# Optimization experiments

Hardware: AMD Instinct MI355X
Metric: run time of the kernel (lower is better)

The kernel has to match this reference:

```python
import jax, jax.numpy as jnp
import numpy as np

B, T, C = 2, 2048, 1024
H = 16
D = C // H  # head_dim = 64


def setup_inputs() -> dict:
    key = jax.random.key(0)
    k1, k2, k3 = jax.random.split(key, 3)
    x = jax.random.normal(k1, (B, T, C), dtype=jnp.float32)
    # torch Linear(C, 3C, bias=False): y = x @ W.T; store transposed weight [C, 3C]
    w_qkv = jax.random.normal(k2, (C, 3 * C), dtype=jnp.float32) * (1.0 / np.sqrt(C))
    w_out = jax.random.normal(k3, (C, C), dtype=jnp.float32) * (1.0 / np.sqrt(C))
    return {"x": x, "w_qkv": w_qkv, "w_out": w_out}


def reference(x, w_qkv, w_out):
    b, t, c = x.shape
    qkv = jnp.einsum('btc,cd->btd', x, w_qkv)          # [B,T,3C]
    q, k, v = jnp.split(qkv, 3, axis=-1)
    # [B,T,C] -> [B,H,T,D]
    def heads(u):
        return u.reshape(b, t, H, D).transpose(0, 2, 1, 3)
    q, k, v = heads(q), heads(k), heads(v)
    scale = 1.0 / np.sqrt(D)
    attn = jnp.einsum('bhqd,bhkd->bhqk', q, k) * scale  # [B,H,T,T]
    causal = jnp.tril(jnp.ones((t, t), dtype=bool))
    attn = jnp.where(causal, attn, -jnp.inf)
    attn = jax.nn.softmax(attn, axis=-1)                # dropout p=0.0 -> identity
    out = jnp.einsum('bhqk,bhkd->bhqd', attn, v)        # [B,H,T,D]
    out = out.transpose(0, 2, 1, 3).reshape(b, t, c)
    return jnp.einsum('btc,co->bto', out, w_out)
```

## Files before the change

kernel.cpp:

```cpp
#include <hip/hip_runtime.h>
#include <hip/hip_bf16.h>
#include <stdint.h>


#define Bv 2
#define Tv 2048
#define Cv 1024
#define Hv 16
#define Dv 64
#define Mv 4096

typedef __attribute__((ext_vector_type(8))) __bf16 bf16x8;
typedef __attribute__((ext_vector_type(4))) __bf16 bf16x4;
typedef __attribute__((ext_vector_type(4))) float f32x4;
typedef __attribute__((ext_vector_type(4))) unsigned short ushort4v;

__device__ __forceinline__ unsigned short f2bs(float f) {
  union { __bf16 h; unsigned short s; } u;
  u.h = (__bf16)f;
  return u.s;
}

__device__ __forceinline__ void gload16(const void* g, void* l) {
  __builtin_amdgcn_global_load_lds(
      (__attribute__((address_space(1))) void*)(uintptr_t)g,
      (__attribute__((address_space(3))) void*)(unsigned int)(uintptr_t)l,
      16, 0, 0);
}

__device__ __forceinline__ bf16x8 ldfrag(const unsigned short* p) {
  return *reinterpret_cast<const bf16x8*>(p);
}
__device__ __forceinline__ bf16x8 ldfragb(const __bf16* p) {
  return *reinterpret_cast<const bf16x8*>(p);
}

__global__ void __launch_bounds__(256) cast_bf16(const float* __restrict__ in,
                                                 unsigned short* __restrict__ out) {
  int i = (blockIdx.x * 256 + threadIdx.x) * 8;
  float4 a = *reinterpret_cast<const float4*>(in + i);
  float4 b = *reinterpret_cast<const float4*>(in + i + 4);
  ushort4v o0, o1;
  o0.x = f2bs(a.x); o0.y = f2bs(a.y); o0.z = f2bs(a.z); o0.w = f2bs(a.w);
  o1.x = f2bs(b.x); o1.y = f2bs(b.y); o1.z = f2bs(b.z); o1.w = f2bs(b.w);
  *reinterpret_cast<ushort4v*>(out + i) = o0;
  *reinterpret_cast<ushort4v*>(out + i + 4) = o1;
}

__global__ void __launch_bounds__(256) transcast(const float* __restrict__ in,
                                                 unsigned short* __restrict__ out,
                                                 int R, int Cc) {
  __shared__ float tile[32][33];
  int c0 = blockIdx.x * 32;
  int r0 = blockIdx.y * 32;
  int tc = threadIdx.x & 31, tr = threadIdx.x >> 5;
#pragma unroll
  for (int i = 0; i < 4; i++)
    tile[tr + i * 8][tc] = in[(size_t)(r0 + tr + i * 8) * Cc + c0 + tc];
  __syncthreads();
#pragma unroll
  for (int i = 0; i < 4; i++)
    out[(size_t)(c0 + tr + i * 8) * R + r0 + tc] = f2bs(tile[tc][tr + i * 8]);
}

template <int EPI>
__global__ void __launch_bounds__(256) gemm128(
    const unsigned short* __restrict__ A, const unsigned short* __restrict__ Bt,
    float* __restrict__ outF, unsigned short* __restrict__ qo,
    unsigned short* __restrict__ ko, unsigned short* __restrict__ vTo, int N) {
  __shared__ unsigned short la[3][4][128][8];
  __shared__ unsigned short lb[3][4][128][8];
  const int K = 1024;
  const int NT = K / 32;
  int mb = blockIdx.y * 128, nb = blockIdx.x * 128;
  int tid = threadIdx.x;
  int l = tid & 63, w = tid >> 6;
  int wr = w >> 1, wc = w & 1;
  int lr = l & 15, lg = l >> 4;
  f32x4 acc[4][4] = {};
  int c0 = tid >> 7, r0 = tid & 127;

  auto STAGE = [&](int t, int buf) {
    int kb = t * 32;
    gload16(A + (size_t)(mb + r0) * K + kb + c0 * 8, &la[buf][c0][r0][0]);
    gload16(A + (size_t)(mb + r0) * K + kb + (c0 + 2) * 8, &la[buf][c0 + 2][r0][0]);
    gload16(Bt + (size_t)(nb + r0) * K + kb + c0 * 8, &lb[buf][c0][r0][0]);
    gload16(Bt + (size_t)(nb + r0) * K + kb + (c0 + 2) * 8, &lb[buf][c0 + 2][r0][0]);
  };
  auto COMPUTE = [&](int buf) {
    bf16x8 af[4], bfr[4];
#pragma unroll
    for (int mi = 0; mi < 4; mi++) af[mi] = ldfrag(&la[buf][lg][wr * 64 + mi * 16 + lr][0]);
#pragma unroll
    for (int ni = 0; ni < 4; ni++) bfr[ni] = ldfrag(&lb[buf][lg][wc * 64 + ni * 16 + lr][0]);
#pragma unroll
    for (int mi = 0; mi < 4; mi++)
#pragma unroll
      for (int ni = 0; ni < 4; ni++)
        acc[mi][ni] = __builtin_amdgcn_mfma_f32_16x16x32_bf16(af[mi], bfr[ni], acc[mi][ni], 0, 0, 0);
  };

  STAGE(0, 0);
  STAGE(1, 1);
  for (int i = 0; i < NT - 1; ++i) {
    asm volatile("s_waitcnt vmcnt(4)" ::: "memory");
    __builtin_amdgcn_s_barrier();
    __builtin_amdgcn_sched_barrier(0);
    if (i + 2 < NT) STAGE(i + 2, (i + 2) % 3);
    COMPUTE(i % 3);
  }
  asm volatile("s_waitcnt vmcnt(0)" ::: "memory");
  __builtin_amdgcn_s_barrier();
  __builtin_amdgcn_sched_barrier(0);
  COMPUTE((NT - 1) % 3);

#pragma unroll
  for (int mi = 0; mi < 4; mi++) {
#pragma unroll
    for (int ni = 0; ni < 4; ni++) {
      int row0 = mb + wr * 64 + mi * 16 + lg * 4;
      int col = nb + wc * 64 + ni * 16 + lr;
      if (EPI == 1) {
#pragma unroll
        for (int r = 0; r < 4; r++)
          outF[(size_t)(row0 + r) * N + col] = acc[mi][ni][r];
      } else {
        int which = col >> 10, cc = col & 1023;
        int h = cc >> 6, d = cc & 63;
        int bb = row0 >> 11, t = row0 & 2047;
        size_t bh = (size_t)bb * Hv + h;
        if (which == 0) {
#pragma unroll
          for (int r = 0; r < 4; r++)
            qo[(bh * Tv + t + r) * Dv + d] = f2bs(acc[mi][ni][r]);
        } else if (which == 1) {
#pragma unroll
          for (int r = 0; r < 4; r++)
            ko[(bh * Tv + t + r) * Dv + d] = f2bs(acc[mi][ni][r]);
        } else {
          ushort4v pk;
#pragma unroll
          for (int r = 0; r < 4; r++) pk[r] = f2bs(acc[mi][ni][r]);
          *reinterpret_cast<ushort4v*>(&vTo[(bh * Dv + d) * Tv + t]) = pk;
        }
      }
    }
  }
}

__global__ void __launch_bounds__(512) flash_attn(
    const unsigned short* __restrict__ Q, const unsigned short* __restrict__ Kk,
    const unsigned short* __restrict__ Vt, unsigned short* __restrict__ O) {
  __shared__ unsigned short lK[2][8][64][8];
  __shared__ unsigned short lV[2][8][64][8];
  __shared__ __bf16 lP[8][16][72];
  int idx = blockIdx.x;
  int p = idx & 255;
  int bh = p & 31;
  int qh = 8 + (p >> 5);
  int qblk = (idx < 256) ? qh : (15 - qh);
  int b = bh >> 4, h = bh & 15;
  int tid = threadIdx.x;
  int l = tid & 63, w = tid >> 6;
  int lr = l & 15, lg = l >> 4;
  const unsigned short* Qp = Q + (size_t)bh * Tv * Dv;
  const unsigned short* Kp = Kk + (size_t)bh * Tv * Dv;
  const unsigned short* Vp = Vt + (size_t)bh * Dv * Tv;
  const float Cs = 0.125f * 1.4426950408889634f;
  const float THRraw = 8.0f / Cs;
  const __bf16 kOne = (__bf16)1.0f;
  const bf16x8 vone = {kOne, kOne, kOne, kOne, kOne, kOne, kOne, kOne};
  int sr = l, sc = w;

  int q0 = qblk * 128;
  int nt = 2 * qblk + 2;
  int qrow = q0 + w * 16 + lr;
  bf16x8 qf0 = ldfrag(&Qp[(size_t)qrow * Dv + lg * 8]);
  bf16x8 qf1 = ldfrag(&Qp[(size_t)qrow * Dv + 32 + lg * 8]);
  f32x4 o[4] = {};
  f32x4 lsum = {0.f, 0.f, 0.f, 0.f};
  float mrow = -1e30f;
  int wlo = q0 + w * 16;

  auto STAGE = [&](int it, int buf) {
    int k0 = it * 64;
    gload16(Kp + (size_t)(k0 + sr) * Dv + sc * 8, &lK[buf][sc][sr][0]);
    gload16(Vp + (size_t)sr * Tv + k0 + sc * 8, &lV[buf][sc][sr][0]);
  };

  STAGE(0, 0);
  int cur = 0;
  for (int it = 0; it < nt; ++it) {
    __syncthreads();
    if (it + 1 < nt) STAGE(it + 1, cur ^ 1);
    int k0 = it * 64;
    if (k0 <= wlo + 15) {
      f32x4 s[4] = {};
#pragma unroll
      for (int j = 0; j < 4; ++j) {
        bf16x8 kf0 = ldfrag(&lK[cur][lg][j * 16 + lr][0]);
        s[j] = __builtin_amdgcn_mfma_f32_16x16x32_bf16(kf0, qf0, s[j], 0, 0, 0);
        bf16x8 kf1 = ldfrag(&lK[cur][4 + lg][j * 16 + lr][0]);
        s[j] = __builtin_amdgcn_mfma_f32_16x16x32_bf16(kf1, qf1, s[j], 0, 0, 0);
      }
      int qg = wlo + lr;
      if (k0 + 63 > wlo) {
#pragma unroll
        for (int j = 0; j < 4; ++j)
#pragma unroll
          for (int r = 0; r < 4; ++r)
            if (k0 + j * 16 + lg * 4 + r > qg) s[j][r] = -1e30f;
      }
      float v = fmaxf(fmaxf(fmaxf(s[0][0], s[0][1]), fmaxf(s[0][2], s[0][3])),
                      fmaxf(fmaxf(s[1][0], s[1][1]), fmaxf(s[1][2], s[1][3])));
      v = fmaxf(v, fmaxf(fmaxf(fmaxf(s[2][0], s[2][1]), fmaxf(s[2][2], s[2][3])),
                         fmaxf(fmaxf(s[3][0], s[3][1]), fmaxf(s[3][2], s[3][3]))));
      v = fmaxf(v, __shfl_xor(v, 16));
      v = fmaxf(v, __shfl_xor(v, 32));
      if (__any(v > mrow + THRraw)) {
        float mn = fmaxf(mrow, v);
        float al = exp2f((mrow - mn) * Cs);
        mrow = mn;
#pragma unroll
        for (int r = 0; r < 4; ++r) {
          float alr = __shfl(al, (l & 48) | (lg * 4 + r));
          lsum[r] *= alr;
#pragma unroll
          for (int nb = 0; nb < 4; ++nb) o[nb][r] *= alr;
        }
      }
#pragma unroll
      for (int j = 0; j < 4; ++j) {
        bf16x4 pk;
#pragma unroll
        for (int r = 0; r < 4; ++r) pk[r] = (__bf16)exp2f((s[j][r] - mrow) * Cs);
        *reinterpret_cast<bf16x4*>(&lP[w][lr][j * 16 + lg * 4]) = pk;
      }
      asm volatile("" ::: "memory");
      f32x4 srow = {0.f, 0.f, 0.f, 0.f};
#pragma unroll
      for (int kk = 0; kk < 2; ++kk) {
        bf16x8 pf = ldfragb(&lP[w][lr][kk * 32 + lg * 8]);
        srow = __builtin_amdgcn_mfma_f32_16x16x32_bf16(pf, vone, srow, 0, 0, 0);
#pragma unroll
        for (int nb = 0; nb < 4; ++nb) {
          bf16x8 vf = ldfrag(&lV[cur][kk * 4 + lg][nb * 16 + lr][0]);
          o[nb] = __builtin_amdgcn_mfma_f32_16x16x32_bf16(pf, vf, o[nb], 0, 0, 0);
        }
      }
      asm volatile("" ::: "memory");
#pragma unroll
      for (int r = 0; r < 4; ++r) lsum[r] += srow[r];
    }
    cur ^= 1;
  }
#pragma unroll
  for (int r = 0; r < 4; ++r) {
    int t = q0 + w * 16 + lg * 4 + r;
    float inv = 1.0f / lsum[r];
    size_t rowbase = ((size_t)b * Tv + t) * Cv + h * Dv;
#pragma unroll
    for (int nb = 0; nb < 4; ++nb)
      O[rowbase + nb * 16 + lr] = f2bs(o[nb][r] * inv);
  }
}

extern "C" void kernel_launch(void* const* d_in, const int* in_sizes, int n_in,
                              void* d_out, int out_size, void* d_ws, size_t ws_size,
                              hipStream_t stream) {
  const float* x = (const float*)d_in[0];
  const float* w_qkv = (const float*)d_in[1];
  const float* w_out = (const float*)d_in[2];
  float* out = (float*)d_out;
  char* ws = (char*)d_ws;
  const size_t MB = 1u << 20;
  unsigned short* xb    = (unsigned short*)(ws + 0);
  unsigned short* wqkvT = (unsigned short*)(ws + 8 * MB);
  unsigned short* woutT = (unsigned short*)(ws + 14 * MB);
  unsigned short* qb    = (unsigned short*)(ws + 16 * MB);
  unsigned short* kb    = (unsigned short*)(ws + 24 * MB);
  unsigned short* vTb   = (unsigned short*)(ws + 32 * MB);
  unsigned short* ab    = (unsigned short*)(ws + 40 * MB);

  cast_bf16<<<dim3(Mv * Cv / (256 * 8)), dim3(256), 0, stream>>>(x, xb);
  transcast<<<dim3(3072 / 32, 1024 / 32), dim3(256), 0, stream>>>(w_qkv, wqkvT, 1024, 3072);
  transcast<<<dim3(1024 / 32, 1024 / 32), dim3(256), 0, stream>>>(w_out, woutT, 1024, 1024);
  gemm128<0><<<dim3(3072 / 128, Mv / 128), dim3(256), 0, stream>>>(
      xb, wqkvT, nullptr, qb, kb, vTb, 3072);
  flash_attn<<<dim3(512), dim3(512), 0, stream>>>(qb, kb, vTb, ab);
  gemm128<1><<<dim3(Cv / 128, Mv / 128), dim3(256), 0, stream>>>(
      ab, woutT, out, nullptr, nullptr, nullptr, Cv);
}
```

Before: 135.9 us.

## Use 256x256 tiled GEMM with 512 threads for QKV projection

```diff
diff --git a/kernel.cpp b/kernel.cpp
--- a/kernel.cpp
+++ b/kernel.cpp
@@ -63,11 +63,90 @@
     out[(size_t)(c0 + tr + i * 8) * R + r0 + tc] = f2bs(tile[tc][tr + i * 8]);
 }
 
-template <int EPI>
+__global__ void __launch_bounds__(512, 1) gemm256_qkv(
+    const unsigned short* __restrict__ A, const unsigned short* __restrict__ Bt,
+    unsigned short* __restrict__ qo, unsigned short* __restrict__ ko,
+    unsigned short* __restrict__ vTo) {
+  __shared__ unsigned short la[2][8][256][8];
+  __shared__ unsigned short lb[2][8][256][8];
+  const int K = 1024;
+  int mb = blockIdx.y * 256, nb = blockIdx.x * 256;
+  int tid = threadIdx.x;
+  int l = tid & 63, w = tid >> 6;
+  int wr = w >> 2, wc = w & 3;
+  int lr = l & 15, lg = l >> 4;
+  f32x4 acc[8][4] = {};
+
+  auto STAGE = [&](int i, int buf) {
+    int kb = i * 64;
+#pragma unroll
+    for (int p = 0; p < 4; ++p) {
+      int slot = tid + 512 * p;
+      int c = slot >> 8, r = slot & 255;
+      gload16(A + (size_t)(mb + r) * K + kb + c * 8, &la[buf][c][r][0]);
+      gload16(Bt + (size_t)(nb + r) * K + kb + c * 8, &lb[buf][c][r][0]);
+    }
+  };
+  auto PHASE = [&](int buf, int ks) {
+    bf16x8 bfr[4];
+#pragma unroll
+    for (int ni = 0; ni < 4; ni++)
+      bfr[ni] = ldfrag(&lb[buf][ks * 4 + lg][wc * 64 + ni * 16 + lr][0]);
+    __builtin_amdgcn_s_setprio(1);
+#pragma unroll
+    for (int mi = 0; mi < 8; mi++) {
+      bf16x8 af = ldfrag(&la[buf][ks * 4 + lg][wr * 128 + mi * 16 + lr][0]);
+#pragma unroll
+      for (int ni = 0; ni < 4; ni++)
+        acc[mi][ni] = __builtin_amdgcn_mfma_f32_16x16x32_bf16(af, bfr[ni], acc[mi][ni], 0, 0, 0);
+    }
+    __builtin_amdgcn_s_setprio(0);
+  };
+
+  STAGE(0, 0);
+  for (int i = 0; i < 16; ++i) {
+    int buf = i & 1;
+    asm volatile("s_waitcnt vmcnt(0)" ::: "memory");
+    __builtin_amdgcn_s_barrier();
+    __builtin_amdgcn_sched_barrier(0);
+    PHASE(buf, 0);
+    __builtin_amdgcn_sched_barrier(0);
+    if (i + 1 < 16) STAGE(i + 1, buf ^ 1);
+    __builtin_amdgcn_sched_barrier(0);
+    PHASE(buf, 1);
+  }
+
+#pragma unroll
+  for (int mi = 0; mi < 8; mi++) {
+#pragma unroll
+    for (int ni = 0; ni < 4; ni++) {
+      int row0 = mb + wr * 128 + mi * 16 + lg * 4;
+      int col = nb + wc * 64 + ni * 16 + lr;
+      int which = col >> 10, cc = col & 1023;
+      int h = cc >> 6, d = cc & 63;
+      int bb = row0 >> 11, t = row0 & 2047;
+      size_t bh = (size_t)bb * Hv + h;
+      if (which == 0) {
+#pragma unroll
+        for (int r = 0; r < 4; r++)
+          qo[(bh * Tv + t + r) * Dv + d] = f2bs(acc[mi][ni][r]);
+      } else if (which == 1) {
+#pragma unroll
+        for (int r = 0; r < 4; r++)
+          ko[(bh * Tv + t + r) * Dv + d] = f2bs(acc[mi][ni][r]);
+      } else {
+        ushort4v pk;
+#pragma unroll
+        for (int r = 0; r < 4; r++) pk[r] = f2bs(acc[mi][ni][r]);
+        *reinterpret_cast<ushort4v*>(&vTo[(bh * Dv + d) * Tv + t]) = pk;
+      }
+    }
+  }
+}
+
 __global__ void __launch_bounds__(256) gemm128(
     const unsigned short* __restrict__ A, const unsigned short* __restrict__ Bt,
-    float* __restrict__ outF, unsigned short* __restrict__ qo,
-    unsigned short* __restrict__ ko, unsigned short* __restrict__ vTo, int N) {
+    float* __restrict__ outF, int N) {
   __shared__ unsigned short la[3][4][128][8];
   __shared__ unsigned short lb[3][4][128][8];
   const int K = 1024;
@@ -120,30 +199,9 @@
     for (int ni = 0; ni < 4; ni++) {
       int row0 = mb + wr * 64 + mi * 16 + lg * 4;
       int col = nb + wc * 64 + ni * 16 + lr;
-      if (EPI == 1) {
-#pragma unroll
-        for (int r = 0; r < 4; r++)
-          outF[(size_t)(row0 + r) * N + col] = acc[mi][ni][r];
-      } else {
-        int which = col >> 10, cc = col & 1023;
-        int h = cc >> 6, d = cc & 63;
-        int bb = row0 >> 11, t = row0 & 2047;
-        size_t bh = (size_t)bb * Hv + h;
-        if (which == 0) {
-#pragma unroll
-          for (int r = 0; r < 4; r++)
-            qo[(bh * Tv + t + r) * Dv + d] = f2bs(acc[mi][ni][r]);
-        } else if (which == 1) {
-#pragma unroll
-          for (int r = 0; r < 4; r++)
-            ko[(bh * Tv + t + r) * Dv + d] = f2bs(acc[mi][ni][r]);
-        } else {
-          ushort4v pk;
-#pragma unroll
-          for (int r = 0; r < 4; r++) pk[r] = f2bs(acc[mi][ni][r]);
-          *reinterpret_cast<ushort4v*>(&vTo[(bh * Dv + d) * Tv + t]) = pk;
-        }
-      }
+#pragma unroll
+      for (int r = 0; r < 4; r++)
+        outF[(size_t)(row0 + r) * N + col] = acc[mi][ni][r];
     }
   }
 }
@@ -285,9 +343,8 @@
   cast_bf16<<<dim3(Mv * Cv / (256 * 8)), dim3(256), 0, stream>>>(x, xb);
   transcast<<<dim3(3072 / 32, 1024 / 32), dim3(256), 0, stream>>>(w_qkv, wqkvT, 1024, 3072);
   transcast<<<dim3(1024 / 32, 1024 / 32), dim3(256), 0, stream>>>(w_out, woutT, 1024, 1024);
-  gemm128<0><<<dim3(3072 / 128, Mv / 128), dim3(256), 0, stream>>>(
-      xb, wqkvT, nullptr, qb, kb, vTb, 3072);
+  gemm256_qkv<<<dim3(3072 / 256, Mv / 256), dim3(512), 0, stream>>>(
+      xb, wqkvT, qb, kb, vTb);
   flash_attn<<<dim3(512), dim3(512), 0, stream>>>(qb, kb, vTb, ab);
-  gemm128<1><<<dim3(Cv / 128, Mv / 128), dim3(256), 0, stream>>>(
-      ab, woutT, out, nullptr, nullptr, nullptr, Cv);
-}
+  gemm128<<<dim3(Cv / 128, Mv / 128), dim3(256), 0, stream>>>(ab, woutT, out, Cv);
+}
```

After: 155.8 us. 14.7% more time.
